# Kernel optimization log

Hardware: AMD Instinct MI355X
Metric: run time of the kernel (lower is better)

The kernel has to match this reference:

```python
import jax, jax.numpy as jnp
import numpy as np

NMS_PRE_MAXSIZE = 4096
NMS_POST_MAXSIZE = 512
NMS_THRESH = 0.7


def setup_inputs() -> dict:
    key = jax.random.key(0)
    k1, k2, k3, k4, k5 = jax.random.split(key, 5)
    B, N, C = 4, 32768, 3
    # realistic 3D boxes: (x, y, z, dx, dy, dz, heading)
    xy = jax.random.uniform(k1, (B, N, 2), dtype=jnp.float32) * 70.0
    z = jax.random.uniform(k2, (B, N, 1), dtype=jnp.float32) * 4.0 - 2.0
    sizes = jax.random.uniform(k3, (B, N, 3), dtype=jnp.float32) * 3.0 + 1.0
    heading = jax.random.uniform(k4, (B, N, 1), dtype=jnp.float32) * 6.2832 - 3.1416
    batch_box_preds = jnp.concatenate([xy, z, sizes, heading], axis=-1)  # (B,N,7)
    batch_cls_preds = jax.random.uniform(k5, (B, N, C), dtype=jnp.float32)  # (B,N,3)
    return {"batch_box_preds": batch_box_preds, "batch_cls_preds": batch_cls_preds}


def _nms_single(boxes, scores, labels):
    # boxes (N,7), scores (N,), labels (N,) int32
    top_s, idx = jax.lax.top_k(scores, NMS_PRE_MAXSIZE)   # sort desc, keep pre-maxsize
    b = boxes[idx]                                        # (PRE,7)
    l = labels[idx]
    # BEV axis-aligned IoU (reference surrogate for the rotated-BEV CUDA IoU kernel)
    x, y, dx, dy = b[:, 0], b[:, 1], b[:, 3], b[:, 4]
    x1, x2 = x - 0.5 * dx, x + 0.5 * dx
    y1, y2 = y - 0.5 * dy, y + 0.5 * dy
    area = dx * dy
    ix = jnp.maximum(0.0, jnp.minimum(x2[:, None], x2[None, :]) - jnp.maximum(x1[:, None], x1[None, :]))
    iy = jnp.maximum(0.0, jnp.minimum(y2[:, None], y2[None, :]) - jnp.maximum(y1[:, None], y1[None, :]))
    inter = ix * iy
    iou = jax.lax.stop_gradient(inter / (area[:, None] + area[None, :] - inter + 1e-6))

    ar = jnp.arange(NMS_PRE_MAXSIZE)

    def body(i, keep):
        sup = (iou[i] > NMS_THRESH) & (ar > i) & keep[i]
        return keep & ~sup

    keep = jax.lax.fori_loop(0, NMS_PRE_MAXSIZE, body, jnp.ones(NMS_PRE_MAXSIZE, bool))

    # pack first NMS_POST_MAXSIZE kept boxes into fixed-size zero-padded outputs
    rank = jnp.cumsum(keep) - 1
    valid = keep & (rank < NMS_POST_MAXSIZE)
    pos = jnp.where(valid, rank, NMS_POST_MAXSIZE)  # invalid -> scratch row
    rois = jnp.zeros((NMS_POST_MAXSIZE + 1, 7), b.dtype).at[pos].set(b)[:NMS_POST_MAXSIZE]
    sc = jnp.zeros((NMS_POST_MAXSIZE + 1,), top_s.dtype).at[pos].set(top_s)[:NMS_POST_MAXSIZE]
    lb = jnp.zeros((NMS_POST_MAXSIZE + 1,), jnp.int32).at[pos].set(l)[:NMS_POST_MAXSIZE]
    return rois, sc, lb


def reference(batch_box_preds, batch_cls_preds):
    # per-box max score / argmax class (torch.max(cls_preds, dim=1) per sample)
    roi_scores_all = jnp.max(batch_cls_preds, axis=-1)                 # (B,N)
    roi_labels_all = jnp.argmax(batch_cls_preds, axis=-1).astype(jnp.int32)
    rois, roi_scores, roi_labels = jax.vmap(_nms_single)(batch_box_preds, roi_scores_all, roi_labels_all)
    return rois, roi_scores, roi_labels + 1  # labels shifted by +1 as in proposal_layer
```

## Files before the change

kernel.cpp:

```cpp
#include <hip/hip_runtime.h>
#include <stdint.h>

#define BB 4
#define NN 32768
#define PRE 4096
#define POST 512
#define NMS_TH 0.7f
#define MIDCAP 8192
#define P1G 16

typedef unsigned long long u64;
typedef unsigned int u32;

__device__ __forceinline__ u32 orderable(float f) {
  u32 u = __float_as_uint(f);
  return (u & 0x80000000u) ? ~u : (u | 0x80000000u);
}
__device__ __forceinline__ float unorderable(u32 o) {
  u32 u = (o & 0x80000000u) ? (o & 0x7fffffffu) : ~o;
  return __uint_as_float(u);
}
__device__ __forceinline__ u32 bucket_of(float s) {
  u32 v = (u32)(s * 2147483648.0f);
  u32 bk = v >> 20;
  return bk > 2047u ? 2047u : bk;
}
__device__ __forceinline__ u64 readlane64(u64 v, int l) {
  u32 lo = (u32)__builtin_amdgcn_readlane((int)(u32)v, l);
  u32 hi = (u32)__builtin_amdgcn_readlane((int)(u32)(v >> 32), l);
  return ((u64)hi << 32) | lo;
}

__global__ void zero_kernel(u32* __restrict__ hist, u32* __restrict__ cnt_mid) {
  int t = blockIdx.x * 256 + threadIdx.x;
  if (t < BB * 2048) hist[t] = 0;
  if (t < BB) cnt_mid[t] = 0;
}

__global__ __launch_bounds__(256) void score_hist_kernel(const float* __restrict__ cls,
                                                         int* __restrict__ labels,
                                                         u64* __restrict__ keys,
                                                         u32* __restrict__ hist) {
  __shared__ u32 lh[2048];
  for (int t = threadIdx.x; t < 2048; t += 256) lh[t] = 0;
  __syncthreads();
  int g = blockIdx.x * 256 + threadIdx.x;
  const float* c = cls + (size_t)g * 3;
  float s = c[0]; int l = 0;
  float c1 = c[1], c2 = c[2];
  if (c1 > s) { s = c1; l = 1; }
  if (c2 > s) { s = c2; l = 2; }
  int n = g & (NN - 1);
  keys[g] = ((u64)orderable(s) << 32) | (u32)(~(u32)n);
  labels[g] = l;
  atomicAdd(&lh[bucket_of(s)], 1u);
  __syncthreads();
  int b = blockIdx.x >> 7;
  for (int t = threadIdx.x; t < 2048; t += 256) {
    u32 v = lh[t];
    if (v) atomicAdd(&hist[b * 2048 + t], v);
  }
}

__global__ __launch_bounds__(256) void select_kernel(const u32* __restrict__ hist,
                                                     u32* __restrict__ selinfo,
                                                     u32* __restrict__ sfxBuf,
                                                     u32* __restrict__ cursor) {
  __shared__ u32 sfx[2048];
  int b = blockIdx.x;
  for (int t = threadIdx.x; t < 2048; t += 256) sfx[t] = hist[b * 2048 + t];
  __syncthreads();
  for (int d = 1; d < 2048; d <<= 1) {
    u32 v[8];
#pragma unroll
    for (int i = 0; i < 8; ++i) {
      int t = threadIdx.x + i * 256;
      v[i] = (t + d < 2048) ? sfx[t + d] : 0;
    }
    __syncthreads();
#pragma unroll
    for (int i = 0; i < 8; ++i) sfx[threadIdx.x + i * 256] += v[i];
    __syncthreads();
  }
  for (int t = threadIdx.x; t < 2048; t += 256) {
    u32 above = (t + 1 < 2048) ? sfx[t + 1] : 0;
    sfxBuf[b * 2048 + t] = sfx[t];
    cursor[b * 2048 + t] = above;
    if (above < PRE && sfx[t] >= PRE) { selinfo[b * 2] = (u32)t; selinfo[b * 2 + 1] = above; }
  }
}

__global__ __launch_bounds__(256) void compact_kernel(const u64* __restrict__ keys,
                                                      const u32* __restrict__ selinfo,
                                                      u32* __restrict__ cursor,
                                                      u64* __restrict__ sel, u64* __restrict__ mid,
                                                      u32* __restrict__ cnt_mid) {
  int g = blockIdx.x * 256 + threadIdx.x;
  int b = g >> 15;
  u64 key = keys[g];
  u32 bk = bucket_of(unorderable((u32)(key >> 32)));
  u32 T = selinfo[b * 2];
  if (bk > T) {
    u32 p = atomicAdd(&cursor[b * 2048 + bk], 1u);
    sel[((size_t)b << 12) + p] = key;
  } else if (bk == T) {
    u32 p = atomicAdd(&cnt_mid[b], 1u);
    if (p < MIDCAP) mid[(size_t)b * MIDCAP + p] = key;
  }
}

__global__ __launch_bounds__(64) void bsort_kernel(u64* __restrict__ sel, u64* __restrict__ mid,
                                                   const u32* __restrict__ sfxBuf,
                                                   const u32* __restrict__ selinfo,
                                                   const u32* __restrict__ cnt_mid) {
  int t = blockIdx.x & 2047;
  int b = blockIdx.x >> 11;
  int lane = threadIdx.x;
  u32 T = selinfo[b * 2];
  u64* selB = sel + ((size_t)b << 12);
  if ((u32)t == T) {
    u32 C1 = selinfo[b * 2 + 1];
    int need = PRE - (int)C1;
    int M = (int)cnt_mid[b]; if (M > MIDCAP) M = MIDCAP;
    u64* midB = mid + (size_t)b * MIDCAP;
    for (int r = 0; r < need; ++r) {
      u64 best = 0; int bi = -1;
      for (int q = lane; q < M; q += 64) {
        u64 v = midB[q];
        if (v > best) { best = v; bi = q; }
      }
#pragma unroll
      for (int d = 32; d > 0; d >>= 1) {
        u64 ob = __shfl_xor(best, d, 64);
        int oi = __shfl_xor(bi, d, 64);
        if (ob > best) { best = ob; bi = oi; }
      }
      if (lane == 0) selB[C1 + r] = best;
      if (bi >= 0 && lane == (bi & 63)) midB[bi] = 0;
    }
    return;
  }
  if ((u32)t < T) return;
  u32 start = (t < 2047) ? sfxBuf[b * 2048 + t + 1] : 0u;
  u32 end = sfxBuf[b * 2048 + t];
  int n = (int)(end - start);
  if (n <= 1) return;
  if (n <= 64) {
    u64 v = (lane < n) ? selB[start + lane] : 0ULL;
#pragma unroll
    for (int k = 2; k <= 64; k <<= 1) {
#pragma unroll
      for (int j = k >> 1; j > 0; j >>= 1) {
        u64 o = __shfl_xor(v, j, 64);
        bool up = ((lane & k) == 0);
        bool first = ((lane & j) == 0);
        u64 mx = v > o ? v : o, mn = v > o ? o : v;
        v = (first == up) ? mx : mn;
      }
    }
    if (lane < n) selB[start + lane] = v;
  } else {
    for (int r = 0; r < n - 1; ++r) {
      u64 best = 0; int bi = -1;
      for (int q = r + lane; q < n; q += 64) {
        u64 v = selB[start + q];
        if (v > best) { best = v; bi = q; }
      }
#pragma unroll
      for (int d = 32; d > 0; d >>= 1) {
        u64 ob = __shfl_xor(best, d, 64);
        int oi = __shfl_xor(bi, d, 64);
        if (ob > best) { best = ob; bi = oi; }
      }
      if (lane == 0) {
        u64 tmp = selB[start + r];
        selB[start + r] = best;
        selB[start + bi] = tmp;
      }
    }
  }
}

__global__ void gather_kernel(const u64* __restrict__ keys, const float* __restrict__ boxes,
                              const int* __restrict__ labels,
                              float* __restrict__ topBox, float4* __restrict__ P,
                              float* __restrict__ AR,
                              float* __restrict__ topS, int* __restrict__ topL) {
  int g = blockIdx.x * blockDim.x + threadIdx.x;
  if (g >= BB * PRE) return;
  int b = g >> 12;
  u64 key = keys[g];
  u32 n = ~(u32)key;
  size_t src = (size_t)b * NN + n;
  const float* bx = boxes + src * 7;
  float x = bx[0], y = bx[1], dx = bx[3], dy = bx[4];
  float* tb = topBox + (size_t)g * 7;
#pragma unroll
  for (int c = 0; c < 7; ++c) tb[c] = bx[c];
  float4 p;
  p.x = x - 0.5f * dx; p.z = x + 0.5f * dx;
  p.y = y - 0.5f * dy; p.w = y + 0.5f * dy;
  P[g] = p;
  AR[g] = dx * dy;
  topS[g] = unorderable((u32)(key >> 32));
  topL[g] = labels[src];
}

__device__ __forceinline__ void mask_tile(int b, int rb, int w, int lane,
                                          const float4* __restrict__ P,
                                          const float* __restrict__ AR,
                                          u64* __restrict__ maskT,
                                          u64* __restrict__ diag) {
  int base = b << 12;
  int row = (rb << 6) + lane;
  float4 rp = P[base + row];
  float rar = AR[base + row];
  const float4* __restrict__ Pcol = P + base + (w << 6);
  const float* __restrict__ ARcol = AR + base + (w << 6);
  u64 bits = 0;
  float margMin = 1.0f;
#pragma unroll 8
  for (int k = 0; k < 64; ++k) {
    float4 cb = Pcol[k];
    float ca = ARcol[k];
    float ix = fminf(rp.z, cb.z) - fmaxf(rp.x, cb.x); ix = fmaxf(0.0f, ix);
    float iy = fminf(rp.w, cb.w) - fmaxf(rp.y, cb.y); iy = fmaxf(0.0f, iy);
    float inter = ix * iy;
    float denom = ((rar + ca) - inter) + 1e-6f;
    float t = 0.7f * denom;
    bits |= ((u64)(inter > t ? 1u : 0u)) << k;
    margMin = fminf(margMin, fabsf(inter - t) - 2e-5f * t);
  }
  if (__any(margMin <= 0.0f)) {
    bits = 0;
    for (int k = 0; k < 64; ++k) {
      float4 cb = Pcol[k];
      float ca = ARcol[k];
      float ix = fminf(rp.z, cb.z) - fmaxf(rp.x, cb.x); ix = fmaxf(0.0f, ix);
      float iy = fminf(rp.w, cb.w) - fmaxf(rp.y, cb.y); iy = fmaxf(0.0f, iy);
      float inter = ix * iy;
      float denom = ((rar + ca) - inter) + 1e-6f;
      bits |= ((u64)(((inter / denom) > NMS_TH) ? 1u : 0u)) << k;
    }
  }
  maskT[((size_t)(b * 64 + w)) * PRE + row] = bits;
  if (w == rb) diag[base + row] = bits;
}

__global__ __launch_bounds__(256) void mask1_kernel(const float4* __restrict__ P,
                                                    const float* __restrict__ AR,
                                                    u64* __restrict__ maskT,
                                                    u64* __restrict__ diag) {
  int b = blockIdx.y;
  int ti = blockIdx.x * 4 + (threadIdx.x >> 6);
  int lane = threadIdx.x & 63;
  int rb = 0;
  while (rb < P1G - 1 && (64 * (rb + 1) - ((rb + 1) * rb) / 2) <= ti) ++rb;
  int w = rb + (ti - (64 * rb - (rb * (rb - 1)) / 2));
  mask_tile(b, rb, w, lane, P, AR, maskT, diag);
}

__global__ __launch_bounds__(256) void mask2_kernel(const float4* __restrict__ P,
                                                    const float* __restrict__ AR,
                                                    u64* __restrict__ maskT,
                                                    u64* __restrict__ diag,
                                                    const u32* __restrict__ doneFlag) {
  int b = blockIdx.y;
  if (doneFlag[b]) return;
  int ti = blockIdx.x * 4 + (threadIdx.x >> 6);
  int lane = threadIdx.x & 63;
  int rr = 0;
  while (rr < 47 && (48 * (rr + 1) - ((rr + 1) * rr) / 2) <= ti) ++rr;
  int rb = rr + P1G;
  int w = rb + (ti - (48 * rr - (rr * (rr - 1)) / 2));
  mask_tile(b, rb, w, lane, P, AR, maskT, diag);
}

__global__ __launch_bounds__(64) void scan_kernel(const u64* __restrict__ maskT,
                                                  const u64* __restrict__ diag,
                                                  const float* __restrict__ topBox,
                                                  const float* __restrict__ topS,
                                                  const int* __restrict__ topL,
                                                  float* __restrict__ out,
                                                  u64* __restrict__ rState,
                                                  u64* __restrict__ kwState,
                                                  u32* __restrict__ nkState,
                                                  u32* __restrict__ doneFlag,
                                                  int phase) {
  __shared__ u64 kwLDS[64];
  int b = blockIdx.x;
  int lane = threadIdx.x;
  if (phase == 1 && doneFlag[b]) return;
  const u64* m = maskT + (size_t)b * 64 * PRE;
  const u64* dg = diag + (size_t)b * PRE;
  u64 r; int nk, gs, ge;
  if (phase == 0) {
    kwLDS[lane] = 0; r = 0; nk = 0; gs = 0; ge = P1G;
  } else {
    kwLDS[lane] = (lane < P1G) ? kwState[b * 64 + lane] : 0;
    r = rState[b * 64 + lane]; nk = nkState[b]; gs = P1G; ge = 64;
  }
  __syncthreads();
  bool done = false;
  u64 d_next = dg[(size_t)gs * 64 + lane];
  for (int g = gs; g < ge; ++g) {
    u64 d_cur = d_next;
    if (g + 1 < ge) d_next = dg[(size_t)(g + 1) * 64 + lane];
    const ulonglong2* mp = (const ulonglong2*)(m + (size_t)lane * PRE + ((size_t)g << 6));
    ulonglong2 rv[32];
#pragma unroll
    for (int q = 0; q < 32; ++q) rv[q] = mp[q];
    u64 sup = readlane64(r, g);
    u64 keep = 0;
#pragma unroll
    for (int k = 0; k < 64; ++k) {
      u64 dk = readlane64(d_cur, k);
      u64 bit = (sup >> k) & 1ULL;
      keep |= (bit ^ 1ULL) << k;
      sup |= (dk & ~((2ULL << k) - 1ULL)) & (bit - 1ULL);
    }
    u64 acc = 0;
#pragma unroll
    for (int q = 0; q < 32; ++q) {
      u64 g0 = 0ULL - ((keep >> (2 * q)) & 1ULL);
      u64 g1 = 0ULL - ((keep >> (2 * q + 1)) & 1ULL);
      acc |= (rv[q].x & g0) | (rv[q].y & g1);
    }
    r |= acc;
    if (lane == 0) kwLDS[g] = keep;
    nk += (int)__popcll(keep);
    if (nk >= POST) { done = true; break; }
  }
  __syncthreads();
  if (phase == 0 && !done) {
    rState[b * 64 + lane] = r;
    if (lane < P1G) kwState[b * 64 + lane] = kwLDS[lane];
    if (lane == 0) { nkState[b] = nk; doneFlag[b] = 0; }
    return;
  }
  if (phase == 0 && lane == 0) doneFlag[b] = 1;
  u64 kw = kwLDS[lane];
  int cnt = __popcll(kw);
  int pfx = cnt;
#pragma unroll
  for (int d = 1; d < 64; d <<= 1) {
    int up = __shfl_up(pfx, d, 64);
    if (lane >= d) pfx += up;
  }
  int total = __shfl(pfx, 63, 64);
  int pos = pfx - cnt;
  float* outR = out;
  float* outS = out + BB * POST * 7;
  float* outL = outS + BB * POST;
  while (kw) {
    int t = __ffsll((long long)kw) - 1;
    kw &= kw - 1;
    if (pos < POST) {
      int i = (lane << 6) + t;
      int g = (b << 9) + pos;
      const float* tb = topBox + ((size_t)(b << 12) + i) * 7;
#pragma unroll
      for (int c = 0; c < 7; ++c) outR[(size_t)g * 7 + c] = tb[c];
      outS[g] = topS[(b << 12) + i];
      outL[g] = (float)(topL[(b << 12) + i] + 1);
    }
    ++pos;
  }
  int fin = total < POST ? total : POST;
  for (int s = fin + lane; s < POST; s += 64) {
    int g = (b << 9) + s;
#pragma unroll
    for (int c = 0; c < 7; ++c) outR[(size_t)g * 7 + c] = 0.0f;
    outS[g] = 0.0f;
    outL[g] = 1.0f;
  }
}

extern "C" void kernel_launch(void* const* d_in, const int* in_sizes, int n_in,
                              void* d_out, int out_size, void* d_ws, size_t ws_size,
                              hipStream_t stream) {
  const float* boxes = (const float*)d_in[0];
  const float* cls   = (const float*)d_in[1];
  float* out = (float*)d_out;

  char* p = (char*)d_ws;
  auto take = [&](size_t bytes) { char* r = p; p += (bytes + 255) & ~(size_t)255; return (void*)r; };
  u64*   keys    = (u64*)  take((size_t)BB * NN * 8);
  int*   labels  = (int*)  take((size_t)BB * NN * 4);
  u32*   hist    = (u32*)  take((size_t)BB * 2048 * 4);
  u32*   selinfo = (u32*)  take((size_t)BB * 2 * 4);
  u32*   sfxBuf  = (u32*)  take((size_t)BB * 2048 * 4);
  u32*   cursor  = (u32*)  take((size_t)BB * 2048 * 4);
  u32*   cnt_mid = (u32*)  take((size_t)BB * 4);
  u64*   sel     = (u64*)  take((size_t)BB * PRE * 8);
  u64*   mid     = (u64*)  take((size_t)BB * MIDCAP * 8);
  float* topBox  = (float*)take((size_t)BB * PRE * 7 * 4);
  float4* Pb     = (float4*)take((size_t)BB * PRE * 16);
  float* AR      = (float*)take((size_t)BB * PRE * 4);
  float* topS    = (float*)take((size_t)BB * PRE * 4);
  int*   topL    = (int*)  take((size_t)BB * PRE * 4);
  u64*   maskT   = (u64*)  take((size_t)BB * 64 * PRE * 8);
  u64*   diagBuf = (u64*)  take((size_t)BB * PRE * 8);
  u64*   rState  = (u64*)  take((size_t)BB * 64 * 8);
  u64*   kwState = (u64*)  take((size_t)BB * 64 * 8);
  u32*   nkState = (u32*)  take((size_t)BB * 4);
  u32*   doneFlg = (u32*)  take((size_t)BB * 4);

  zero_kernel<<<32, 256, 0, stream>>>(hist, cnt_mid);
  score_hist_kernel<<<BB * NN / 256, 256, 0, stream>>>(cls, labels, keys, hist);
  select_kernel<<<BB, 256, 0, stream>>>(hist, selinfo, sfxBuf, cursor);
  compact_kernel<<<BB * NN / 256, 256, 0, stream>>>(keys, selinfo, cursor, sel, mid, cnt_mid);
  bsort_kernel<<<BB * 2048, 64, 0, stream>>>(sel, mid, sfxBuf, selinfo, cnt_mid);
  gather_kernel<<<(BB * PRE + 255) / 256, 256, 0, stream>>>(sel, boxes, labels,
                                                            topBox, Pb, AR, topS, topL);
  mask1_kernel<<<dim3(226, BB), 256, 0, stream>>>(Pb, AR, maskT, diagBuf);
  scan_kernel<<<BB, 64, 0, stream>>>(maskT, diagBuf, topBox, topS, topL, out,
                                     rState, kwState, nkState, doneFlg, 0);
  mask2_kernel<<<dim3(294, BB), 256, 0, stream>>>(Pb, AR, maskT, diagBuf, doneFlg);
  scan_kernel<<<BB, 64, 0, stream>>>(maskT, diagBuf, topBox, topS, topL, out,
                                     rState, kwState, nkState, doneFlg, 1);
}
```

Before: 103.8 us.

## Fuse gather into bucket sort and skip serial diag scan when empty

The separate gather kernel is removed. Each bucket-sort block now gathers boxes, corners, areas, scores and labels for the slice it just sorted, which saves one launch and one pass over the sorted keys. In the scan kernel, a ballot checks whether the 64x64 diagonal block has any suppression bits. When it has none, keep is computed as the complement of sup instead of running the 64-step serial loop. Mask row loads are also moved inline into the accumulation loop and launch bounds are tightened to one block. Risks: the gather now runs inside small 64-thread blocks with uneven per-block work, and the serial-sort block for the threshold bucket also has to gather its whole range.

```diff
diff --git a/kernel.cpp b/kernel.cpp
--- a/kernel.cpp
+++ b/kernel.cpp
@@ -112,12 +112,21 @@
 __global__ __launch_bounds__(64) void bsort_kernel(u64* __restrict__ sel, u64* __restrict__ mid,
                                                    const u32* __restrict__ sfxBuf,
                                                    const u32* __restrict__ selinfo,
-                                                   const u32* __restrict__ cnt_mid) {
+                                                   const u32* __restrict__ cnt_mid,
+                                                   const float* __restrict__ boxes,
+                                                   const int* __restrict__ labels,
+                                                   float* __restrict__ topBox,
+                                                   float4* __restrict__ P,
+                                                   float* __restrict__ AR,
+                                                   float* __restrict__ topS,
+                                                   int* __restrict__ topL) {
   int t = blockIdx.x & 2047;
   int b = blockIdx.x >> 11;
   int lane = threadIdx.x;
   u32 T = selinfo[b * 2];
+  if ((u32)t < T) return;
   u64* selB = sel + ((size_t)b << 12);
+  u32 start, end;
   if ((u32)t == T) {
     u32 C1 = selinfo[b * 2 + 1];
     int need = PRE - (int)C1;
@@ -138,72 +147,65 @@
       if (lane == 0) selB[C1 + r] = best;
       if (bi >= 0 && lane == (bi & 63)) midB[bi] = 0;
     }
-    return;
-  }
-  if ((u32)t < T) return;
-  u32 start = (t < 2047) ? sfxBuf[b * 2048 + t + 1] : 0u;
-  u32 end = sfxBuf[b * 2048 + t];
-  int n = (int)(end - start);
-  if (n <= 1) return;
-  if (n <= 64) {
-    u64 v = (lane < n) ? selB[start + lane] : 0ULL;
-#pragma unroll
-    for (int k = 2; k <= 64; k <<= 1) {
-#pragma unroll
-      for (int j = k >> 1; j > 0; j >>= 1) {
-        u64 o = __shfl_xor(v, j, 64);
-        bool up = ((lane & k) == 0);
-        bool first = ((lane & j) == 0);
-        u64 mx = v > o ? v : o, mn = v > o ? o : v;
-        v = (first == up) ? mx : mn;
+    start = C1; end = PRE;
+  } else {
+    start = (t < 2047) ? sfxBuf[b * 2048 + t + 1] : 0u;
+    end = sfxBuf[b * 2048 + t];
+    int n = (int)(end - start);
+    if (n > 64) {
+      for (int r = 0; r < n - 1; ++r) {
+        u64 best = 0; int bi = -1;
+        for (int q = r + lane; q < n; q += 64) {
+          u64 v = selB[start + q];
+          if (v > best) { best = v; bi = q; }
+        }
+#pragma unroll
+        for (int d = 32; d > 0; d >>= 1) {
+          u64 ob = __shfl_xor(best, d, 64);
+          int oi = __shfl_xor(bi, d, 64);
+          if (ob > best) { best = ob; bi = oi; }
+        }
+        if (lane == 0) {
+          u64 tmp = selB[start + r];
+          selB[start + r] = best;
+          selB[start + bi] = tmp;
+        }
       }
-    }
-    if (lane < n) selB[start + lane] = v;
-  } else {
-    for (int r = 0; r < n - 1; ++r) {
-      u64 best = 0; int bi = -1;
-      for (int q = r + lane; q < n; q += 64) {
-        u64 v = selB[start + q];
-        if (v > best) { best = v; bi = q; }
+    } else if (n > 1) {
+      u64 v = (lane < n) ? selB[start + lane] : 0ULL;
+#pragma unroll
+      for (int k = 2; k <= 64; k <<= 1) {
+#pragma unroll
+        for (int j = k >> 1; j > 0; j >>= 1) {
+          u64 o = __shfl_xor(v, j, 64);
+          bool up = ((lane & k) == 0);
+          bool first = ((lane & j) == 0);
+          u64 mx = v > o ? v : o, mn = v > o ? o : v;
+          v = (first == up) ? mx : mn;
+        }
       }
-#pragma unroll
-      for (int d = 32; d > 0; d >>= 1) {
-        u64 ob = __shfl_xor(best, d, 64);
-        int oi = __shfl_xor(bi, d, 64);
-        if (ob > best) { best = ob; bi = oi; }
-      }
-      if (lane == 0) {
-        u64 tmp = selB[start + r];
-        selB[start + r] = best;
-        selB[start + bi] = tmp;
-      }
-    }
-  }
-}
-
-__global__ void gather_kernel(const u64* __restrict__ keys, const float* __restrict__ boxes,
-                              const int* __restrict__ labels,
-                              float* __restrict__ topBox, float4* __restrict__ P,
-                              float* __restrict__ AR,
-                              float* __restrict__ topS, int* __restrict__ topL) {
-  int g = blockIdx.x * blockDim.x + threadIdx.x;
-  if (g >= BB * PRE) return;
-  int b = g >> 12;
-  u64 key = keys[g];
-  u32 n = ~(u32)key;
-  size_t src = (size_t)b * NN + n;
-  const float* bx = boxes + src * 7;
-  float x = bx[0], y = bx[1], dx = bx[3], dy = bx[4];
-  float* tb = topBox + (size_t)g * 7;
-#pragma unroll
-  for (int c = 0; c < 7; ++c) tb[c] = bx[c];
-  float4 p;
-  p.x = x - 0.5f * dx; p.z = x + 0.5f * dx;
-  p.y = y - 0.5f * dy; p.w = y + 0.5f * dy;
-  P[g] = p;
-  AR[g] = dx * dy;
-  topS[g] = unorderable((u32)(key >> 32));
-  topL[g] = labels[src];
+      if (lane < n) selB[start + lane] = v;
+    }
+  }
+  __builtin_amdgcn_s_waitcnt(0);
+  for (u32 pos = start + lane; pos < end; pos += 64) {
+    u64 key = selB[pos];
+    u32 n = ~(u32)key;
+    size_t src = (size_t)b * NN + n;
+    const float* bx = boxes + src * 7;
+    float x = bx[0], y = bx[1], dx = bx[3], dy = bx[4];
+    size_t gidx = ((size_t)b << 12) + pos;
+    float* tb = topBox + gidx * 7;
+#pragma unroll
+    for (int c = 0; c < 7; ++c) tb[c] = bx[c];
+    float4 p;
+    p.x = x - 0.5f * dx; p.z = x + 0.5f * dx;
+    p.y = y - 0.5f * dy; p.w = y + 0.5f * dy;
+    P[gidx] = p;
+    AR[gidx] = dx * dy;
+    topS[gidx] = unorderable((u32)(key >> 32));
+    topL[gidx] = labels[src];
+  }
 }
 
 __device__ __forceinline__ void mask_tile(int b, int rb, int w, int lane,
@@ -276,17 +278,17 @@
   mask_tile(b, rb, w, lane, P, AR, maskT, diag);
 }
 
-__global__ __launch_bounds__(64) void scan_kernel(const u64* __restrict__ maskT,
-                                                  const u64* __restrict__ diag,
-                                                  const float* __restrict__ topBox,
-                                                  const float* __restrict__ topS,
-                                                  const int* __restrict__ topL,
-                                                  float* __restrict__ out,
-                                                  u64* __restrict__ rState,
-                                                  u64* __restrict__ kwState,
-                                                  u32* __restrict__ nkState,
-                                                  u32* __restrict__ doneFlag,
-                                                  int phase) {
+__global__ __launch_bounds__(64, 1) void scan_kernel(const u64* __restrict__ maskT,
+                                                     const u64* __restrict__ diag,
+                                                     const float* __restrict__ topBox,
+                                                     const float* __restrict__ topS,
+                                                     const int* __restrict__ topL,
+                                                     float* __restrict__ out,
+                                                     u64* __restrict__ rState,
+                                                     u64* __restrict__ kwState,
+                                                     u32* __restrict__ nkState,
+                                                     u32* __restrict__ doneFlag,
+                                                     int phase) {
   __shared__ u64 kwLDS[64];
   int b = blockIdx.x;
   int lane = threadIdx.x;
@@ -306,25 +308,29 @@
   for (int g = gs; g < ge; ++g) {
     u64 d_cur = d_next;
     if (g + 1 < ge) d_next = dg[(size_t)(g + 1) * 64 + lane];
+    u64 sup = readlane64(r, g);
+    u64 keep;
+    u64 anyd = __ballot(d_cur != 0ULL);
+    if (anyd == 0ULL) {
+      keep = ~sup;
+    } else {
+      keep = 0;
+#pragma unroll
+      for (int k = 0; k < 64; ++k) {
+        u64 dk = readlane64(d_cur, k);
+        u64 bit = (sup >> k) & 1ULL;
+        keep |= (bit ^ 1ULL) << k;
+        sup |= (dk & ~((2ULL << k) - 1ULL)) & (bit - 1ULL);
+      }
+    }
     const ulonglong2* mp = (const ulonglong2*)(m + (size_t)lane * PRE + ((size_t)g << 6));
-    ulonglong2 rv[32];
-#pragma unroll
-    for (int q = 0; q < 32; ++q) rv[q] = mp[q];
-    u64 sup = readlane64(r, g);
-    u64 keep = 0;
-#pragma unroll
-    for (int k = 0; k < 64; ++k) {
-      u64 dk = readlane64(d_cur, k);
-      u64 bit = (sup >> k) & 1ULL;
-      keep |= (bit ^ 1ULL) << k;
-      sup |= (dk & ~((2ULL << k) - 1ULL)) & (bit - 1ULL);
-    }
     u64 acc = 0;
 #pragma unroll
     for (int q = 0; q < 32; ++q) {
+      ulonglong2 v = mp[q];
       u64 g0 = 0ULL - ((keep >> (2 * q)) & 1ULL);
       u64 g1 = 0ULL - ((keep >> (2 * q + 1)) & 1ULL);
-      acc |= (rv[q].x & g0) | (rv[q].y & g1);
+      acc |= (v.x & g0) | (v.y & g1);
     }
     r |= acc;
     if (lane == 0) kwLDS[g] = keep;
@@ -410,9 +416,8 @@
   score_hist_kernel<<<BB * NN / 256, 256, 0, stream>>>(cls, labels, keys, hist);
   select_kernel<<<BB, 256, 0, stream>>>(hist, selinfo, sfxBuf, cursor);
   compact_kernel<<<BB * NN / 256, 256, 0, stream>>>(keys, selinfo, cursor, sel, mid, cnt_mid);
-  bsort_kernel<<<BB * 2048, 64, 0, stream>>>(sel, mid, sfxBuf, selinfo, cnt_mid);
-  gather_kernel<<<(BB * PRE + 255) / 256, 256, 0, stream>>>(sel, boxes, labels,
-                                                            topBox, Pb, AR, topS, topL);
+  bsort_kernel<<<BB * 2048, 64, 0, stream>>>(sel, mid, sfxBuf, selinfo, cnt_mid,
+                                             boxes, labels, topBox, Pb, AR, topS, topL);
   mask1_kernel<<<dim3(226, BB), 256, 0, stream>>>(Pb, AR, maskT, diagBuf);
   scan_kernel<<<BB, 64, 0, stream>>>(maskT, diagBuf, topBox, topS, topL, out,
                                      rState, kwState, nkState, doneFlg, 0);
```

Result: slower. 106.4 us (+2.5%).
